# Optimization experiments

Hardware: AMD Instinct MI355X
Metric: run time of the kernel (lower is better)

## Reference

```python
import jax, jax.numpy as jnp
import numpy as np

ETA = 0.5
R_CUTOFF = 6.0
ZETA = 0.6
LAMDA = 0.8
RS = 1.0
SPECIAL_ATOM = 8  # atom index routed to elem2 net


def _af(x):
    return 1.0 / (1.0 + x * x)


def _mlp(g, w1, b1, w2, b2, w3, b3):
    h = _af(g @ w1.T + b1)
    h = _af(h @ w2.T + b2)
    return h @ w3.T + b3  # [N,1]


def setup_inputs() -> dict:
    key = jax.random.key(0)
    ks = jax.random.split(key, 13)
    N = 384
    x = jax.random.normal(ks[0], (N, 3), dtype=jnp.float32) * 2.0
    def lin(kw, kb, fout, fin):
        w = jax.random.normal(kw, (fout, fin), dtype=jnp.float32) * (1.0 / np.sqrt(fin))
        b = jax.random.normal(kb, (fout,), dtype=jnp.float32) * 0.1
        return w, b
    w1a, b1a = lin(ks[1], ks[2], 40, 2)
    w2a, b2a = lin(ks[3], ks[4], 40, 40)
    w3a, b3a = lin(ks[5], ks[6], 1, 40)
    w1b, b1b = lin(ks[7], ks[8], 40, 2)
    w2b, b2b = lin(ks[9], ks[10], 40, 40)
    w3b, b3b = lin(ks[11], ks[12], 1, 40)
    return {"x": x,
            "w1a": w1a, "b1a": b1a, "w2a": w2a, "b2a": b2a, "w3a": w3a, "b3a": b3a,
            "w1b": w1b, "b1b": b1b, "w2b": w2b, "b2b": b2b, "w3b": w3b, "b3b": b3b}


def _descriptors(x):
    N = x.shape[0]
    eye = jnp.eye(N, dtype=bool)
    diff = x[:, None, :] - x[None, :, :]           # [N,N,3]
    D2 = jnp.sum(diff * diff, axis=-1)             # [N,N]
    D = jnp.sqrt(jnp.where(eye, 1.0, D2))
    D = jnp.where(eye, 0.0, D)
    # cutoff function (hard 0 beyond R_cutoff), zeroed on diagonal
    fc = jnp.where((D <= R_CUTOFF) & (~eye), 0.5 * (jnp.cos(np.pi * D / R_CUTOFF) + 1.0), 0.0)
    # radial symmetry function per atom i
    rad = jnp.sum(jnp.exp(-ETA * (D - RS) ** 2) * fc, axis=1)  # [N]
    # angular: sum over triplets j<k, j!=i, k!=i
    A = jnp.exp(-ETA * D2) * fc                    # [N,N], zero on diagonal
    Gm = x @ x.T                                   # Gram matrix
    gd = jnp.diag(Gm)
    # dot(Rij, Rki) with Rij = x_i - x_j, Rki = x_k - x_i
    dot = Gm[:, None, :] - gd[:, None, None] - Gm[None, :, :] + Gm[:, :, None]  # [N,N,N] (i,j,k)
    denom = D[:, :, None] * D[:, None, :]          # |Rij| * |Rki|
    cos_theta = dot / jnp.where(denom > 0, denom, 1.0)
    term1 = jnp.maximum(1.0 + LAMDA * cos_theta, 1e-6) ** ZETA
    # A[i,j] * A[j,k] * A[k,i]; diag-zero A kills i==j and i==k terms
    term2 = A[:, :, None] * A[None, :, :] * A[:, None, :]
    tri = jnp.triu(jnp.ones((N, N), dtype=jnp.float32), k=1)[None, :, :]  # j < k
    ang = (2.0 ** (1.0 - ZETA)) * jnp.sum(term1 * term2 * tri, axis=(1, 2))  # [N]
    return jnp.stack([ang, rad], axis=-1)          # [N,2], order matches Gi=[ang, rad]


def reference(x, w1a, b1a, w2a, b2a, w3a, b3a, w1b, b1b, w2b, b2b, w3b, b3b):
    G = _descriptors(x)
    q1 = _mlp(G, w1a, b1a, w2a, b2a, w3a, b3a)[:, 0]
    q2 = _mlp(G, w1b, b1b, w2b, b2b, w3b, b3b)[:, 0]
    idx = jnp.arange(x.shape[0])
    return jnp.where(idx == SPECIAL_ATOM, q2, q1)  # [N]
```

## Files before the change

### kernel.cpp

```cpp
#include <hip/hip_runtime.h>
#include <math.h>

#define N 384
#define JC 8
#define JPC (N / JC)

__device__ __forceinline__ float wave_reduce(float v) {
#pragma unroll
    for (int o = 32; o > 0; o >>= 1) v += __shfl_down(v, o, 64);
    return v;
}

__global__ void pair_kernel(const float* __restrict__ x, float* __restrict__ A,
                            float* __restrict__ rad, float* __restrict__ ang) {
    const int i = blockIdx.x;
    const int t = threadIdx.x;
    const float xi0 = x[3 * i + 0], xi1 = x[3 * i + 1], xi2 = x[3 * i + 2];
    float racc = 0.0f;
    for (int j = t; j < N; j += blockDim.x) {
        float dx = xi0 - x[3 * j + 0];
        float dy = xi1 - x[3 * j + 1];
        float dz = xi2 - x[3 * j + 2];
        float d2 = dx * dx + dy * dy + dz * dz;
        float a = 0.0f, r = 0.0f;
        if (j != i) {
            float d = sqrtf(d2);
            if (d <= 6.0f) {
                float fc = 0.5f * (__cosf(0.52359877559829887f * d) + 1.0f);
                a = __expf(-0.5f * d2) * fc;
                float dm = d - 1.0f;
                r = __expf(-0.5f * dm * dm) * fc;
            }
        }
        A[i * N + j] = a;
        racc += r;
    }
    __shared__ float red[2];
    float v = wave_reduce(racc);
    int lane = t & 63, w = t >> 6;
    if (lane == 0) red[w] = v;
    __syncthreads();
    if (t == 0) {
        rad[i] = red[0] + red[1];
        ang[i] = 0.0f;
    }
}

__global__ __launch_bounds__(128) void ang_kernel(const float* __restrict__ x,
                                                  const float* __restrict__ A,
                                                  float* __restrict__ ang) {
    const int i = blockIdx.x;
    const int t = threadIdx.x;
    __shared__ float4 sh[N];

    const float xi0 = x[3 * i + 0], xi1 = x[3 * i + 1], xi2 = x[3 * i + 2];
    for (int j = t; j < N; j += 128) {
        float dx = xi0 - x[3 * j + 0];
        float dy = xi1 - x[3 * j + 1];
        float dz = xi2 - x[3 * j + 2];
        float d2 = dx * dx + dy * dy + dz * dz;
        float inv = (j == i) ? 0.0f : rsqrtf(d2);
        sh[j] = make_float4(dx * inv, dy * inv, dz * inv, A[i * N + j]);
    }
    __syncthreads();

    float4 f0 = sh[t], f1 = sh[t + 128], f2 = sh[t + 256];
    const float k0x = -0.8f * f0.x, k0y = -0.8f * f0.y, k0z = -0.8f * f0.z, kA0 = f0.w;
    const float k1x = -0.8f * f1.x, k1y = -0.8f * f1.y, k1z = -0.8f * f1.z, kA1 = f1.w;
    const float k2x = -0.8f * f2.x, k2y = -0.8f * f2.y, k2z = -0.8f * f2.z, kA2 = f2.w;

    const int j0 = blockIdx.y * JPC;
    const float* Ar = A + j0 * N;
    float a0 = Ar[t], a1 = Ar[t + 128], a2 = Ar[t + 256];
    float acc = 0.0f;

    for (int j = j0; j < j0 + JPC; ++j) {
        Ar += N;
        float n0 = Ar[t];
        float n1 = Ar[t + 128];
        float n2 = Ar[t + 256];
        float4 J = sh[j];
        if (__builtin_amdgcn_readfirstlane(__float_as_uint(J.w)) != 0u) {
            float b0 = fmaxf(fmaf(J.x, k0x, fmaf(J.y, k0y, fmaf(J.z, k0z, 1.0f))), 1e-6f);
            float b1 = fmaxf(fmaf(J.x, k1x, fmaf(J.y, k1y, fmaf(J.z, k1z, 1.0f))), 1e-6f);
            float b2 = fmaxf(fmaf(J.x, k2x, fmaf(J.y, k2y, fmaf(J.z, k2z, 1.0f))), 1e-6f);
            float p0 = __expf(0.6f * __logf(b0));
            float p1 = __expf(0.6f * __logf(b1));
            float p2 = __expf(0.6f * __logf(b2));
            float s = fmaf(p0, a0 * kA0, fmaf(p1, a1 * kA1, p2 * (a2 * kA2)));
            acc = fmaf(J.w, s, acc);
        }
        a0 = n0; a1 = n1; a2 = n2;
    }

    __shared__ float red[2];
    float v = wave_reduce(acc);
    int lane = t & 63, w = t >> 6;
    if (lane == 0) red[w] = v;
    __syncthreads();
    if (t == 0) atomicAdd(&ang[i], red[0] + red[1]);
}

#define WSTRIDE 1804
__global__ __launch_bounds__(64) void mlp_kernel(
    const float* __restrict__ ang, const float* __restrict__ rad,
    float* __restrict__ out,
    const float* w1a, const float* b1a, const float* w2a, const float* b2a,
    const float* w3a, const float* b3a, const float* w1b, const float* b1b,
    const float* w2b, const float* b2b, const float* w3b, const float* b3b) {
    __shared__ __align__(16) float W[2 * WSTRIDE];
    const int t = threadIdx.x;
    {
        const float* srcs[12] = {w1a, b1a, w2a, b2a, w3a, b3a,
                                 w1b, b1b, w2b, b2b, w3b, b3b};
        const int ns[6] = {80, 40, 1600, 40, 40, 1};
        const int offs[6] = {0, 80, 120, 1720, 1760, 1800};
        for (int s = 0; s < 12; ++s) {
            const int base = (s / 6) * WSTRIDE + offs[s % 6];
            const int n4 = ns[s % 6] >> 2;
            const float4* src4 = (const float4*)srcs[s];
            float4* dst4 = (float4*)(W + base);
            for (int q = t; q < n4; q += 64) dst4[q] = src4[q];
        }
        if (t == 0) {
            W[1800] = b3a[0];
            W[WSTRIDE + 1800] = b3b[0];
        }
    }
    __syncthreads();

    const int atom = blockIdx.x * 16 + (t >> 2);
    const int net = (t >> 1) & 1;
    const int half = t & 1;
    const float* P = W + net * WSTRIDE;

    const float g0 = 0.6597539553864471f * ang[atom];
    const float g1 = rad[atom];

    float h1[40];
#pragma unroll
    for (int u = 0; u < 40; ++u) {
        float z = fmaf(P[2 * u], g0, fmaf(P[2 * u + 1], g1, P[80 + u]));
        h1[u] = 1.0f / fmaf(z, z, 1.0f);
    }

    float acc = half ? 0.0f : P[1800];
    const int v0 = half * 20;
    for (int v2 = v0; v2 < v0 + 20; ++v2) {
        const float4* row = (const float4*)(P + 120 + v2 * 40);
        float z0 = P[1720 + v2], z1 = 0.0f, z2 = 0.0f, z3 = 0.0f;
#pragma unroll
        for (int q = 0; q < 10; ++q) {
            float4 r = row[q];
            z0 = fmaf(r.x, h1[4 * q + 0], z0);
            z1 = fmaf(r.y, h1[4 * q + 1], z1);
            z2 = fmaf(r.z, h1[4 * q + 2], z2);
            z3 = fmaf(r.w, h1[4 * q + 3], z3);
        }
        float z = (z0 + z1) + (z2 + z3);
        float h = 1.0f / fmaf(z, z, 1.0f);
        acc = fmaf(P[1760 + v2], h, acc);
    }
    acc += __shfl_down(acc, 1, 64);

    if (half == 0 && net == ((atom == 8) ? 1 : 0)) out[atom] = acc;
}

extern "C" void kernel_launch(void* const* d_in, const int* in_sizes, int n_in,
                              void* d_out, int out_size, void* d_ws, size_t ws_size,
                              hipStream_t stream) {
    const float* x = (const float*)d_in[0];
    const float* w1a = (const float*)d_in[1];
    const float* b1a = (const float*)d_in[2];
    const float* w2a = (const float*)d_in[3];
    const float* b2a = (const float*)d_in[4];
    const float* w3a = (const float*)d_in[5];
    const float* b3a = (const float*)d_in[6];
    const float* w1b = (const float*)d_in[7];
    const float* b1b = (const float*)d_in[8];
    const float* w2b = (const float*)d_in[9];
    const float* b2b = (const float*)d_in[10];
    const float* w3b = (const float*)d_in[11];
    const float* b3b = (const float*)d_in[12];
    float* out = (float*)d_out;

    float* ws = (float*)d_ws;
    float* A = ws;
    float* rad = ws + N * N;
    float* ang = ws + N * N + N;

    hipLaunchKernelGGL(pair_kernel, dim3(N), dim3(128), 0, stream, x, A, rad, ang);
    hipLaunchKernelGGL(ang_kernel, dim3(N, JC), dim3(128), 0, stream, x, A, ang);
    hipLaunchKernelGGL(mlp_kernel, dim3(24), dim3(64), 0, stream,
                       ang, rad, out,
                       w1a, b1a, w2a, b2a, w3a, b3a,
                       w1b, b1b, w2b, b2b, w3b, b3b);
}
```

Before: 127.4 us.

## Compact neighbor lists and restrict angular triplet loop to significant neighbors

```diff
diff --git a/kernel.cpp b/kernel.cpp
--- a/kernel.cpp
+++ b/kernel.cpp
@@ -2,8 +2,7 @@
 #include <math.h>
 
 #define N 384
-#define JC 8
-#define JPC (N / JC)
+#define EPSA 1e-5f
 
 __device__ __forceinline__ float wave_reduce(float v) {
 #pragma unroll
@@ -11,94 +10,127 @@
     return v;
 }
 
-__global__ void pair_kernel(const float* __restrict__ x, float* __restrict__ A,
-                            float* __restrict__ rad, float* __restrict__ ang) {
+__global__ __launch_bounds__(128) void pair_kernel(
+    const float* __restrict__ x, float* __restrict__ A,
+    float4* __restrict__ nbr4, int* __restrict__ nbrJ, int* __restrict__ cnt,
+    float* __restrict__ rad, float* __restrict__ ang) {
     const int i = blockIdx.x;
     const int t = threadIdx.x;
+    const int lane = t & 63, w = t >> 6;
     const float xi0 = x[3 * i + 0], xi1 = x[3 * i + 1], xi2 = x[3 * i + 2];
+
     float racc = 0.0f;
-    for (int j = t; j < N; j += blockDim.x) {
+    float4 val[3];
+    int keep[3];
+#pragma unroll
+    for (int r = 0; r < 3; ++r) {
+        const int j = t + 128 * r;
         float dx = xi0 - x[3 * j + 0];
         float dy = xi1 - x[3 * j + 1];
         float dz = xi2 - x[3 * j + 2];
         float d2 = dx * dx + dy * dy + dz * dz;
-        float a = 0.0f, r = 0.0f;
+        float a = 0.0f, rr = 0.0f, inv = 0.0f;
         if (j != i) {
             float d = sqrtf(d2);
             if (d <= 6.0f) {
                 float fc = 0.5f * (__cosf(0.52359877559829887f * d) + 1.0f);
                 a = __expf(-0.5f * d2) * fc;
                 float dm = d - 1.0f;
-                r = __expf(-0.5f * dm * dm) * fc;
+                rr = __expf(-0.5f * dm * dm) * fc;
             }
+            inv = rsqrtf(d2);
         }
         A[i * N + j] = a;
-        racc += r;
-    }
+        racc += rr;
+        val[r] = make_float4(dx * inv, dy * inv, dz * inv, a);
+        keep[r] = (a > EPSA) ? 1 : 0;
+    }
+
+    __shared__ int bcnt[6], bbase[6];
+    int pfx[3];
+#pragma unroll
+    for (int r = 0; r < 3; ++r) {
+        unsigned long long m = __ballot(keep[r]);
+        pfx[r] = __popcll(m & ((1ull << lane) - 1ull));
+        if (lane == 0) bcnt[w + 2 * r] = __popcll(m);
+    }
+    __syncthreads();
+    if (t == 0) {
+        int s = 0;
+#pragma unroll
+        for (int c = 0; c < 6; ++c) { bbase[c] = s; s += bcnt[c]; }
+        cnt[i] = s;
+        ang[i] = 0.0f;
+    }
+    __syncthreads();
+#pragma unroll
+    for (int r = 0; r < 3; ++r) {
+        if (keep[r]) {
+            const int slot = bbase[w + 2 * r] + pfx[r];
+            nbr4[i * N + slot] = val[r];
+            nbrJ[i * N + slot] = t + 128 * r;
+        }
+    }
+
     __shared__ float red[2];
     float v = wave_reduce(racc);
-    int lane = t & 63, w = t >> 6;
     if (lane == 0) red[w] = v;
     __syncthreads();
-    if (t == 0) {
-        rad[i] = red[0] + red[1];
-        ang[i] = 0.0f;
-    }
-}
-
-__global__ __launch_bounds__(128) void ang_kernel(const float* __restrict__ x,
-                                                  const float* __restrict__ A,
-                                                  float* __restrict__ ang) {
+    if (t == 0) rad[i] = red[0] + red[1];
+}
+
+__global__ __launch_bounds__(256) void ang_kernel(
+    const float* __restrict__ A, const float4* __restrict__ nbr4,
+    const int* __restrict__ nbrJ, const int* __restrict__ cnt,
+    float* __restrict__ ang) {
     const int i = blockIdx.x;
+    const int kc = blockIdx.y >> 2;
+    const int jc = blockIdx.y & 3;
     const int t = threadIdx.x;
-    __shared__ float4 sh[N];
-
-    const float xi0 = x[3 * i + 0], xi1 = x[3 * i + 1], xi2 = x[3 * i + 2];
-    for (int j = t; j < N; j += 128) {
-        float dx = xi0 - x[3 * j + 0];
-        float dy = xi1 - x[3 * j + 1];
-        float dz = xi2 - x[3 * j + 2];
-        float d2 = dx * dx + dy * dy + dz * dz;
-        float inv = (j == i) ? 0.0f : rsqrtf(d2);
-        sh[j] = make_float4(dx * inv, dy * inv, dz * inv, A[i * N + j]);
-    }
-    __syncthreads();
-
-    float4 f0 = sh[t], f1 = sh[t + 128], f2 = sh[t + 256];
-    const float k0x = -0.8f * f0.x, k0y = -0.8f * f0.y, k0z = -0.8f * f0.z, kA0 = f0.w;
-    const float k1x = -0.8f * f1.x, k1y = -0.8f * f1.y, k1z = -0.8f * f1.z, kA1 = f1.w;
-    const float k2x = -0.8f * f2.x, k2y = -0.8f * f2.y, k2z = -0.8f * f2.z, kA2 = f2.w;
-
-    const int j0 = blockIdx.y * JPC;
-    const float* Ar = A + j0 * N;
-    float a0 = Ar[t], a1 = Ar[t + 128], a2 = Ar[t + 256];
+    const int n = cnt[i];
+    if (kc * 256 >= n) return;
+
+    const int qn = (n + 3) >> 2;
+    const int js = jc * qn;
+    const int je = min(js + qn, n);
+    if (js >= je) return;
+
+    __shared__ float4 sh4[96];
+    __shared__ int shJ[96];
+    for (int s = js + t; s < je; s += 256) {
+        sh4[s - js] = nbr4[i * N + s];
+        shJ[s - js] = nbrJ[i * N + s];
+    }
+
+    const int ks = kc * 256 + t;
+    const int valid = ks < n;
+    float4 K = valid ? nbr4[i * N + ks] : make_float4(0.f, 0.f, 0.f, 0.f);
+    const int kcol = valid ? nbrJ[i * N + ks] : 0;
+    const float kx = -0.8f * K.x, ky = -0.8f * K.y, kz = -0.8f * K.z, kA = K.w;
+    __syncthreads();
+
     float acc = 0.0f;
-
-    for (int j = j0; j < j0 + JPC; ++j) {
-        Ar += N;
-        float n0 = Ar[t];
-        float n1 = Ar[t + 128];
-        float n2 = Ar[t + 256];
-        float4 J = sh[j];
-        if (__builtin_amdgcn_readfirstlane(__float_as_uint(J.w)) != 0u) {
-            float b0 = fmaxf(fmaf(J.x, k0x, fmaf(J.y, k0y, fmaf(J.z, k0z, 1.0f))), 1e-6f);
-            float b1 = fmaxf(fmaf(J.x, k1x, fmaf(J.y, k1y, fmaf(J.z, k1z, 1.0f))), 1e-6f);
-            float b2 = fmaxf(fmaf(J.x, k2x, fmaf(J.y, k2y, fmaf(J.z, k2z, 1.0f))), 1e-6f);
-            float p0 = __expf(0.6f * __logf(b0));
-            float p1 = __expf(0.6f * __logf(b1));
-            float p2 = __expf(0.6f * __logf(b2));
-            float s = fmaf(p0, a0 * kA0, fmaf(p1, a1 * kA1, p2 * (a2 * kA2)));
-            acc = fmaf(J.w, s, acc);
-        }
-        a0 = n0; a1 = n1; a2 = n2;
-    }
-
-    __shared__ float red[2];
+    int jo = __builtin_amdgcn_readfirstlane(shJ[0]);
+    float a = A[jo * N + kcol];
+    for (int s = js; s < je; ++s) {
+        float an = 0.0f;
+        if (s + 1 < je) {
+            int jn = __builtin_amdgcn_readfirstlane(shJ[s - js + 1]);
+            an = A[jn * N + kcol];
+        }
+        float4 J = sh4[s - js];
+        float b = fmaxf(fmaf(J.x, kx, fmaf(J.y, ky, fmaf(J.z, kz, 1.0f))), 1e-6f);
+        float p = __expf(0.6f * __logf(b));
+        acc = fmaf(J.w * a, p, acc);
+        a = an;
+    }
+    acc *= kA;
+
+    __shared__ float red[4];
     float v = wave_reduce(acc);
-    int lane = t & 63, w = t >> 6;
-    if (lane == 0) red[w] = v;
-    __syncthreads();
-    if (t == 0) atomicAdd(&ang[i], red[0] + red[1]);
+    if ((t & 63) == 0) red[t >> 6] = v;
+    __syncthreads();
+    if (t == 0) atomicAdd(&ang[i], red[0] + red[1] + red[2] + red[3]);
 }
 
 #define WSTRIDE 1804
@@ -186,11 +218,16 @@
 
     float* ws = (float*)d_ws;
     float* A = ws;
-    float* rad = ws + N * N;
-    float* ang = ws + N * N + N;
-
-    hipLaunchKernelGGL(pair_kernel, dim3(N), dim3(128), 0, stream, x, A, rad, ang);
-    hipLaunchKernelGGL(ang_kernel, dim3(N, JC), dim3(128), 0, stream, x, A, ang);
+    float4* nbr4 = (float4*)(ws + 147456);
+    int* nbrJ = (int*)(ws + 147456 + 4 * 147456);
+    float* rad = ws + 147456 * 6;
+    float* ang = rad + 384;
+    int* cnt = (int*)(ang + 384);
+
+    hipLaunchKernelGGL(pair_kernel, dim3(N), dim3(128), 0, stream,
+                       x, A, nbr4, nbrJ, cnt, rad, ang);
+    hipLaunchKernelGGL(ang_kernel, dim3(N, 8), dim3(256), 0, stream,
+                       A, nbr4, nbrJ, cnt, ang);
     hipLaunchKernelGGL(mlp_kernel, dim3(24), dim3(64), 0, stream,
                        ang, rad, out,
                        w1a, b1a, w2a, b2a, w3a, b3a,
```

After: 128.3 us. About the same (+0.7%).
